# Optimization experiments

Hardware: AMD Instinct MI355X
Metric: run time of the kernel (lower is better)

Reference implementation:

```python
import jax, jax.numpy as jnp
import numpy as np
import math

HID = 1024      # opt.hidden_dim
NH = 8          # num_heads (hardcoded in module)
HD = HID // NH  # indiv_head_dim = 128
G = 16          # opt.group_num
GD = HID // G   # per-group dim = 64
FEAT = 1024     # opt.feature_dim
V, T = 8, 256   # videos x frames
E = 256         # number of events
L = 64          # max_att_len (clip window)
N = 384         # expanded event_num
WAVE = 10000.0


def setup_inputs() -> dict:
    rng = np.random.RandomState(0)
    key = jax.random.key(0)
    ks = jax.random.split(key, 12)

    feats = jax.random.normal(ks[0], (V * T, FEAT), dtype=jnp.float32)

    # ragged clip spans -> dense gather idx + mask (the Basic_Encoder loop)
    starts = rng.randint(0, V * T - L, size=(E,))
    clip_gather_idx = jnp.asarray(starts[:, None] + np.arange(L)[None, :], dtype=jnp.int32)
    lens = rng.randint(8, L + 1, size=(E,))
    clip_mask = jnp.asarray((np.arange(L)[None, :] < lens[:, None]).astype(np.float32))

    # event_seq_idx expansion: rows -> event ids, block-diagonal mask
    expand_idx = jnp.asarray(rng.randint(0, E, size=(N,)), dtype=jnp.int32)
    block_mask = np.zeros((N, N), dtype=np.float32)
    pos = 0
    while pos < N:
        b = min(int(rng.randint(8, 49)), N - pos)
        block_mask[pos:pos + b, pos:pos + b] = 1.0
        pos += b
    block_mask = jnp.asarray(block_mask)

    # normalized timestamps (start < end, in [0,1])
    s = rng.uniform(0.0, 0.8, size=(N, 1)).astype(np.float32)
    e = s + rng.uniform(0.02, 0.2, size=(N, 1)).astype(np.float32)
    bbox = jnp.asarray(np.concatenate([s, e], axis=1))

    sc = 1.0 / math.sqrt(HID)
    scd = 1.0 / math.sqrt(HD)
    Wpre = jax.random.normal(ks[1], (HID, FEAT), dtype=jnp.float32) * sc
    bpre = jnp.zeros((HID,), dtype=jnp.float32)
    Wq = jax.random.normal(ks[2], (NH, HD, HD), dtype=jnp.float32) * scd
    bq = jnp.zeros((NH, HD), dtype=jnp.float32)
    Wk = jax.random.normal(ks[3], (NH, HD, HD), dtype=jnp.float32) * scd
    bk = jnp.zeros((NH, HD), dtype=jnp.float32)
    Wv = jax.random.normal(ks[4], (NH, HD, HD), dtype=jnp.float32) * scd
    bv = jnp.zeros((NH, HD), dtype=jnp.float32)
    Wp1 = jax.random.normal(ks[5], (HID, HID), dtype=jnp.float32) * sc
    bp1 = jnp.zeros((HID,), dtype=jnp.float32)
    Wp2 = jax.random.normal(ks[6], (G, HID), dtype=jnp.float32) * sc
    bp2 = jnp.zeros((G,), dtype=jnp.float32)

    return dict(feats=feats, clip_gather_idx=clip_gather_idx, clip_mask=clip_mask,
                expand_idx=expand_idx, block_mask=block_mask, bbox=bbox,
                Wpre=Wpre, bpre=bpre, Wq=Wq, bq=bq, Wk=Wk, bk=bk, Wv=Wv, bv=bv,
                Wp1=Wp1, bp1=bp1, Wp2=Wp2, bp2=bp2)


def _sinusoid(x, feat_dim):
    # extract_position_embedding: x [..., P] -> [..., P*feat_dim/2*2] reshaped to feat_dim per row
    fr = jnp.arange(feat_dim // 4, dtype=x.dtype)
    dim_mat = WAVE ** (4.0 / feat_dim * fr)              # (feat_dim/4,)
    div = (100.0 * x)[..., None] / dim_mat               # (..., P, feat_dim/4)
    return jnp.concatenate([jnp.sin(div), jnp.cos(div)], axis=-1)


def reference(feats, clip_gather_idx, clip_mask, expand_idx, block_mask, bbox,
              Wpre, bpre, Wq, bq, Wk, bk, Wv, bv, Wp1, bp1, Wp2, bp2):
    # ---- clip-level pooling (Basic_Encoder.get_clip_level_feats + mean) ----
    clip_feats = feats[clip_gather_idx] * clip_mask[..., None]          # (E, L, FEAT)
    event = clip_feats.sum(1) / (clip_mask.sum(1, keepdims=True) + 1e-5)  # (E, FEAT)
    event = jax.nn.relu(event @ Wpre.T + bpre)                          # pre_map (dropout=eval)

    # ---- expand per event_seq_idx ----
    x = event[expand_idx]                                               # (N, HID)

    # ---- 8 per-head q/k/v maps, split into G groups ----
    xh = x.reshape(N, NH, HD)
    def proj(W, b):
        y = jnp.einsum('nhd,hed->nhe', xh, W) + b                       # (N, NH, HD)
        return y.reshape(N, G, GD).transpose(1, 0, 2)                   # (G, N, GD)
    q, k, v = proj(Wq, bq), proj(Wk, bk), proj(Wv, bv)
    scores = jnp.einsum('gnd,gmd->gnm', q, k) / math.sqrt(GD)           # (G, N, N)

    # ---- position branch: pairwise geometric relation bias ----
    start, end = bbox[:, 0:1], bbox[:, 1:2]                             # (N,1)
    center = 0.5 * (start + end)
    length = jnp.maximum(end - start, 0.1)
    dc = (center - center.T) / length
    dl = jnp.log(length.T / length)
    pm = jnp.stack([dc, dl], axis=2)                                    # (N, N, 2)
    emb = _sinusoid(pm, HID).reshape(N, N, HID)                         # (N, N, HID)
    pos = jax.nn.relu(emb @ Wp1.T + bp1)                                # pair_pos_fc1
    pos = jax.nn.relu(pos @ Wp2.T + bp2)                                # pair_pos_fc2 -> (N, N, G)
    pos_bias = jnp.log(jnp.clip(pos, 1e-6)).transpose(2, 0, 1)          # (G, N, N)

    scores = scores + pos_bias
    scores = jnp.where(block_mask[None] > 0, scores, -1e9)
    att = jax.nn.softmax(scores, axis=-1)                               # (G, N, N)
    out = jnp.einsum('gnm,gmd->gnd', att, v)                            # (G, N, GD)
    out = out.transpose(1, 0, 2).reshape(N, HID)

    # ---- per-event 100-dim temporal position embedding ----
    e100 = _sinusoid(bbox, 100).reshape(N, 100)

    return jnp.concatenate([x, out, e100], axis=-1)                     # (N, 2*HID + 100)
```

## Files before the change

### kernel.cpp

```cpp
#include <hip/hip_runtime.h>
#include <hip/hip_bf16.h>

typedef unsigned short u16;
typedef _Float16 h16;
typedef __attribute__((ext_vector_type(8))) h16 h8;
typedef __attribute__((ext_vector_type(8))) u16 us8;
typedef __attribute__((ext_vector_type(4))) u16 us4;
typedef __attribute__((ext_vector_type(4))) float f4;

#define DEVFN __device__ __forceinline__

constexpr int kN = 384;
constexpr int kL = 64;
constexpr int kMaxP = kN * 48;
constexpr int kOutCols = 2148;
constexpr float kLoScale = 2048.f;
constexpr float kLoInv = 1.f / 2048.f;

union HU { h16 h; u16 u; };
DEVFN u16 f2h(float f) { HU c; c.h = (h16)f; return c.u; }
DEVFN float h2f(u16 b) { HU c; c.u = b; return (float)c.h; }

DEVFN f4 mfma16h(h8 a, h8 b, f4 c) {
  return __builtin_amdgcn_mfma_f32_16x16x32_f16(a, b, c, 0, 0, 0);
}

DEVFN h8 pack8h(float4 x0, float4 x1) {
  h8 a;
  a[0] = (h16)x0.x; a[1] = (h16)x0.y; a[2] = (h16)x0.z; a[3] = (h16)x0.w;
  a[4] = (h16)x1.x; a[5] = (h16)x1.y; a[6] = (h16)x1.z; a[7] = (h16)x1.w;
  return a;
}

DEVFN void fsincos(float ang, float& s, float& c) {
  float n = rintf(ang * 0.15915494309189535f);
  const float PI2_HI = 6.2831854820251465f;
  const float PI2_LO = -1.7484555e-07f;
  float r = fmaf(-n, PI2_HI, ang);
  r = fmaf(-n, PI2_LO, r);
  s = __sinf(r);
  c = __cosf(r);
}

__global__ __launch_bounds__(256) void k_front(
    const float* __restrict__ Wp1, u16* __restrict__ W1H, u16* __restrict__ W1L,
    const float* __restrict__ Wp2, u16* __restrict__ W2H, u16* __restrict__ W2L,
    const float* __restrict__ Wpre, u16* __restrict__ WpreH,
    const float* __restrict__ Wq, u16* __restrict__ WqH,
    const float* __restrict__ Wk, u16* __restrict__ WkH,
    const float* __restrict__ Wv, u16* __restrict__ WvH,
    const float* __restrict__ bm, int* __restrict__ row_start, int* __restrict__ row_len,
    const float* __restrict__ feats, const int* __restrict__ gidx,
    const float* __restrict__ cmask, float* __restrict__ mean,
    float* __restrict__ bias_acc) {
  int bid = blockIdx.x, t = threadIdx.x;
  if (bid < 512) {
    const int nW1 = 1048576, nW2 = 16384, nPre = 1048576, nQ = 131072;
    const int tot = nW1 + nW2 + nPre + 3 * nQ;
    for (int i = bid * 256 + t; i < tot; i += 512 * 256) {
      if (i < nW1) {
        float x = Wp1[i]; u16 h = f2h(x);
        W1H[i] = h; W1L[i] = f2h((x - h2f(h)) * kLoScale);
      } else if (i < nW1 + nW2) {
        int j = i - nW1; float x = Wp2[j]; u16 h = f2h(x);
        W2H[j] = h; W2L[j] = f2h((x - h2f(h)) * kLoScale);
      } else if (i < nW1 + nW2 + nPre) {
        int j = i - nW1 - nW2; WpreH[j] = f2h(Wpre[j]);
      } else {
        int j = i - nW1 - nW2 - nPre;
        int a = j / nQ, r = j % nQ;
        const float* s = (a == 0) ? Wq : (a == 1) ? Wk : Wv;
        u16* d = (a == 0) ? WqH : (a == 1) ? WkH : WvH;
        d[r] = f2h(s[r]);
      }
    }
  } else if (bid < 608) {
    int w = t >> 6, lane = t & 63;
    int i = (bid - 512) * 4 + w;
    int mn = kN, mx = -1;
    #pragma unroll
    for (int jb = 0; jb < kN; jb += 64) {
      float m = bm[(size_t)i * kN + jb + lane];
      if (m > 0.f) { mn = min(mn, jb + lane); mx = max(mx, jb + lane); }
    }
    #pragma unroll
    for (int off = 32; off > 0; off >>= 1) {
      mn = min(mn, __shfl_xor(mn, off));
      mx = max(mx, __shfl_xor(mx, off));
    }
    if (lane == 0) { row_start[i] = mn; row_len[i] = mx - mn + 1; }
  } else if (bid < 864) {
    int e = bid - 608;
    float4 a = {0.f, 0.f, 0.f, 0.f};
    float ms = 0.f;
    for (int l = 0; l < kL; ++l) {
      float m = cmask[e * kL + l];
      ms += m;
      if (m > 0.f) {
        float4 v = *(const float4*)(feats + (size_t)gidx[e * kL + l] * 1024 + t * 4);
        a.x += v.x; a.y += v.y; a.z += v.z; a.w += v.w;
      }
    }
    float inv = 1.f / (ms + 1e-5f);
    float4 o = {a.x * inv, a.y * inv, a.z * inv, a.w * inv};
    *(float4*)(mean + (size_t)e * 1024 + t * 4) = o;
  } else {
    float4 z = {0.f, 0.f, 0.f, 0.f};
    for (int i4 = (bid - 864) * 256 + t; i4 < kMaxP * 16 / 4; i4 += 48 * 256)
      *(float4*)(bias_acc + (size_t)i4 * 4) = z;
  }
}

__global__ __launch_bounds__(64) void k_scan(const int* __restrict__ row_len,
                                             int* __restrict__ row_off,
                                             int* __restrict__ Ptr) {
  int lane = threadIdx.x;
  int s[6], tot = 0;
  #pragma unroll
  for (int r = 0; r < 6; ++r) { s[r] = tot; tot += row_len[lane * 6 + r]; }
  int run = tot;
  #pragma unroll
  for (int off = 1; off < 64; off <<= 1) {
    int u = __shfl_up(run, off);
    if (lane >= off) run += u;
  }
  int excl = run - tot;
  #pragma unroll
  for (int r = 0; r < 6; ++r) row_off[lane * 6 + r] = excl + s[r];
  if (lane == 63) Ptr[0] = excl + tot;
}

__global__ __launch_bounds__(64) void k_fill(const int* __restrict__ row_start,
                                             const int* __restrict__ row_len,
                                             const int* __restrict__ row_off,
                                             int* __restrict__ pair_i,
                                             int* __restrict__ pair_j) {
  int i = blockIdx.x, lane = threadIdx.x;
  int s = row_start[i], len = row_len[i], off = row_off[i];
  if (lane < len) { pair_i[off + lane] = i; pair_j[off + lane] = s + lane; }
}

__global__ __launch_bounds__(256) void k_mid(
    const int* __restrict__ Ptr, const int* __restrict__ row_start,
    const int* __restrict__ row_off, const float* __restrict__ bbox,
    u16* __restrict__ ehi, u16* __restrict__ elo,
    const float* __restrict__ mean, const u16* __restrict__ WpreH,
    const float* __restrict__ bpre, float* __restrict__ event) {
  int bid = blockIdx.x, t = threadIdx.x;
  if (bid < 9216) {
    int P = Ptr[0];
    int Pc = (P + 127) & ~127;
    if (bid * 2 >= Pc) return;
    __shared__ double As[16], Bs[16];
    __shared__ int roff[384], rstart[384];
    const double kCd = -13.287712379549449 / 256.0;
    if (t < 16) As[t] = exp2(kCd * (double)(t * 16));
    else if (t < 32) Bs[t - 16] = exp2(kCd * (double)(t - 16));
    for (int k = t; k < 384; k += 256) { roff[k] = row_off[k]; rstart[k] = row_start[k]; }
    __syncthreads();
    int p = bid * 2 + (t >> 7);
    int u = t & 127;
    int hseg = u >> 6;
    int f0 = (u & 63) * 4;
    size_t ob = (size_t)p * 1024 + hseg * 512 + f0;
    if (p >= P) {
      us4 z = {0, 0, 0, 0};
      *(us4*)(ehi + ob) = z; *(us4*)(ehi + ob + 256) = z;
      *(us4*)(elo + ob) = z; *(us4*)(elo + ob + 256) = z;
      return;
    }
    int lo = 0, hi = 383;
    while (lo < hi) { int md = (lo + hi + 1) >> 1; if (roff[md] <= p) lo = md; else hi = md - 1; }
    int pi = lo, pj = rstart[lo] + (p - roff[lo]);
    double s0 = bbox[pi * 2], e0 = bbox[pi * 2 + 1];
    double s1 = bbox[pj * 2], e1 = bbox[pj * 2 + 1];
    double li = fmax(e0 - s0, 0.1), lj = fmax(e1 - s1, 0.1);
    double x = hseg ? log(lj / li) : (0.5 * (s0 + e0) - 0.5 * (s1 + e1)) / li;
    double x100 = 100.0 * x;
    const double INV2PI = 0.15915494309189535;
    const double TWOPI  = 6.283185307179586;
    us4 sh_, sl_, ch_, cl_;
    #pragma unroll
    for (int j = 0; j < 4; ++j) {
      int f = f0 + j;
      double ang = x100 * (As[f >> 4] * Bs[f & 15]);
      double nn = rint(ang * INV2PI);
      float rf = (float)fma(-nn, TWOPI, ang);
      float sv = __sinf(rf), cv = __cosf(rf);
      u16 hs = f2h(sv); sh_[j] = hs; sl_[j] = f2h((sv - h2f(hs)) * kLoScale);
      u16 hc = f2h(cv); ch_[j] = hc; cl_[j] = f2h((cv - h2f(hc)) * kLoScale);
    }
    *(us4*)(ehi + ob) = sh_; *(us4*)(ehi + ob + 256) = ch_;
    *(us4*)(elo + ob) = sl_; *(us4*)(elo + ob + 256) = cl_;
  } else {
    int b2 = bid - 9216;
    int mt = b2 >> 4, nc = b2 & 15;
    int w = t >> 6, lane = t & 63, lr = lane & 15, lg = lane >> 4;
    f4 acc = {};
    const float* arow = mean + (size_t)(mt * 16 + lr) * 1024;
    #pragma unroll
    for (int ks = 0; ks < 32; ++ks) {
      const float* ap = arow + ks * 32 + lg * 8;
      h8 a = pack8h(*(const float4*)ap, *(const float4*)(ap + 4));
      h8 b = *(const h8*)(WpreH + (size_t)(nc * 64 + w * 16 + lr) * 1024 + ks * 32 + lg * 8);
      acc = mfma16h(a, b, acc);
    }
    #pragma unroll
    for (int r = 0; r < 4; ++r) {
      int row = mt * 16 + lg * 4 + r, cn = nc * 64 + w * 16 + lr;
      event[(size_t)row * 1024 + cn] = fmaxf(acc[r] + bpre[cn], 0.f);
    }
  }
}

__global__ __launch_bounds__(256, 2) void k_main(
    const int* __restrict__ Ptr, const u16* __restrict__ ehi, const u16* __restrict__ elo,
    const u16* __restrict__ W1h, const u16* __restrict__ W1l, const float* __restrict__ bias1,
    const u16* __restrict__ W2h, const u16* __restrict__ W2l, float* __restrict__ bias_acc,
    const float* __restrict__ event, const int* __restrict__ eidx,
    const u16* __restrict__ WqH, const float* __restrict__ bq,
    const u16* __restrict__ WkH, const float* __restrict__ bk,
    const u16* __restrict__ WvH, const float* __restrict__ bv,
    float* __restrict__ qb, float* __restrict__ kbuf, float* __restrict__ vbuf,
    int pos_on) {
  __shared__ u16 lds[2][4][4096];
  int bid = blockIdx.x, tid = threadIdx.x;
  if (bid < 1152) {
    if (!pos_on) return;
    int P = Ptr[0];
    int mb = bid % 144, nb = bid / 144;
    if (mb * 128 >= P) return;
    int w = tid >> 6, lane = tid & 63;
    int lr = lane & 15, lg = lane >> 4;
    int srow[2], scol[2];
    #pragma unroll
    for (int cc = 0; cc < 2; ++cc) {
      int c = w * 2 + cc;
      int d = c * 1024 + lane * 16;
      int b = d ^ (((((d >> 6) & 3)) ^ ((d >> 8) & 3)) << 4);
      srow[cc] = b >> 6;
      scol[cc] = b & 63;
    }
    const u16* planes[4] = {ehi, elo, W1h, W1l};
    int rb0 = mb * 128, rb1 = nb * 128;
    auto stage = [&](int buf, int k0) {
      #pragma unroll
      for (int t = 0; t < 4; ++t) {
        int rbase = (t < 2) ? rb0 : rb1;
        #pragma unroll
        for (int cc = 0; cc < 2; ++cc) {
          int c = w * 2 + cc;
          const char* src = (const char*)(planes[t] + (size_t)(rbase + srow[cc]) * 1024 + k0) + scol[cc];
          char* dst = (char*)&lds[buf][t][0] + c * 1024;
          __builtin_amdgcn_global_load_lds(
              (const __attribute__((address_space(1))) char*)src,
              (__attribute__((address_space(3))) char*)dst, 16, 0, 0);
        }
      }
    };
    stage(0, 0);
    f4 aH[4][4] = {}, aL[4][4] = {};
    int wm = (w >> 1) * 64, wn = (w & 1) * 64;
    int sl = (lg ^ (lr & 3) ^ ((lr >> 2) & 3)) << 4;
    __syncthreads();
    for (int kt = 0; kt < 32; ++kt) {
      int cur = kt & 1;
      if (kt < 31) stage(cur ^ 1, (kt + 1) * 32);
      h8 ah[4], al[4], bh[4], bl[4];
      #pragma unroll
      for (int mt = 0; mt < 4; ++mt) {
        int ad = (wm + mt * 16 + lr) * 64 + sl;
        ah[mt] = *(const h8*)((const char*)&lds[cur][0][0] + ad);
        al[mt] = *(const h8*)((const char*)&lds[cur][1][0] + ad);
      }
      #pragma unroll
      for (int nt = 0; nt < 4; ++nt) {
        int ad = (wn + nt * 16 + lr) * 64 + sl;
        bh[nt] = *(const h8*)((const char*)&lds[cur][2][0] + ad);
        bl[nt] = *(const h8*)((const char*)&lds[cur][3][0] + ad);
      }
      #pragma unroll
      for (int mt = 0; mt < 4; ++mt)
        #pragma unroll
        for (int nt = 0; nt < 4; ++nt) {
          aH[mt][nt] = mfma16h(ah[mt], bh[nt], aH[mt][nt]);
          aL[mt][nt] = mfma16h(al[mt], bh[nt], aL[mt][nt]);
          aL[mt][nt] = mfma16h(ah[mt], bl[nt], aL[mt][nt]);
        }
      __syncthreads();
    }
    float* zq = (float*)&lds[0][0][0] + w * 4096;
    #pragma unroll
    for (int mt = 0; mt < 4; ++mt)
      #pragma unroll
      for (int nt = 0; nt < 4; ++nt)
        #pragma unroll
        for (int r = 0; r < 4; ++r) {
          int pl = mt * 16 + lg * 4 + r;
          int nl = nt * 16 + lr;
          float z1 = aH[mt][nt][r] + aL[mt][nt][r] * kLoInv + bias1[nb * 128 + wn + nl];
          zq[pl * 64 + (nl ^ ((pl & 7) << 3))] = fmaxf(z1, 0.f);
        }
    __syncthreads();
    f4 c2h[4], c2l[4];
    #pragma unroll
    for (int i = 0; i < 4; ++i) { c2h[i] = f4{}; c2l[i] = f4{}; }
    #pragma unroll
    for (int mt2 = 0; mt2 < 4; ++mt2) {
      #pragma unroll
      for (int kc = 0; kc < 2; ++kc) {
        int pl = mt2 * 16 + lr;
        int n0 = kc * 32 + lg * 8;
        const float* rp = zq + pl * 64 + (n0 ^ ((pl & 7) << 3));
        float4 v0 = *(const float4*)rp;
        float4 v1 = *(const float4*)(rp + 4);
        h8 ah2, al2;
        #pragma unroll
        for (int j = 0; j < 4; ++j) {
          h16 h0 = (h16)v0[j]; ah2[j] = h0;     al2[j] = (h16)((v0[j] - (float)h0) * kLoScale);
          h16 h1 = (h16)v1[j]; ah2[4 + j] = h1; al2[4 + j] = (h16)((v1[j] - (float)h1) * kLoScale);
        }
        int ng = nb * 128 + wn + n0;
        h8 bh2 = *(const h8*)(W2h + lr * 1024 + ng);
        h8 bl2 = *(const h8*)(W2l + lr * 1024 + ng);
        c2h[mt2] = mfma16h(ah2, bh2, c2h[mt2]);
        c2l[mt2] = mfma16h(al2, bh2, c2l[mt2]);
        c2l[mt2] = mfma16h(ah2, bl2, c2l[mt2]);
      }
    }
    #pragma unroll
    for (int mt2 = 0; mt2 < 4; ++mt2)
      #pragma unroll
      for (int r = 0; r < 4; ++r) {
        int p = mb * 128 + wm + mt2 * 16 + lg * 4 + r;
        if (p < P)
          atomicAdd(&bias_acc[(size_t)p * 16 + lr], c2h[mt2][r] + c2l[mt2][r] * kLoInv);
      }
  } else {
    int b2 = bid - 1152;
    int z = b2 / 192, r2 = b2 % 192, mt = r2 >> 3, h = r2 & 7;
    int w = tid >> 6, lane = tid & 63, lr = lane & 15, lg = lane >> 4;
    const u16* W = (z == 0) ? WqH : (z == 1) ? WkH : WvH;
    const float* bias = (z == 0) ? bq : (z == 1) ? bk : bv;
    float* out = (z == 0) ? qb : (z == 1) ? kbuf : vbuf;
    int row = mt * 16 + lr;
    const float* arow = event + (size_t)eidx[row] * 1024 + h * 128;
    f4 acc[2] = {};
    #pragma unroll
    for (int ks = 0; ks < 4; ++ks) {
      const float* ap = arow + ks * 32 + lg * 8;
      h8 a = pack8h(*(const float4*)ap, *(const float4*)(ap + 4));
      #pragma unroll
      for (int n2 = 0; n2 < 2; ++n2) {
        int nt = w * 2 + n2;
        h8 b = *(const h8*)(W + h * 16384 + (nt * 16 + lr) * 128 + ks * 32 + lg * 8);
        acc[n2] = mfma16h(a, b, acc[n2]);
      }
    }
    #pragma unroll
    for (int n2 = 0; n2 < 2; ++n2)
      #pragma unroll
      for (int r = 0; r < 4; ++r) {
        int rn = mt * 16 + lg * 4 + r, e = (w * 2 + n2) * 16 + lr;
        out[(size_t)rn * 1024 + h * 128 + e] = acc[n2][r] + bias[h * 128 + e];
      }
  }
}

__global__ __launch_bounds__(64) void k_att(const float* __restrict__ q,
                                            const float* __restrict__ kk,
                                            const float* __restrict__ vv,
                                            const float* __restrict__ bias_acc,
                                            const float* __restrict__ bias2,
                                            const int* __restrict__ row_start,
                                            const int* __restrict__ row_len,
                                            const int* __restrict__ row_off,
                                            const float* __restrict__ event,
                                            const int* __restrict__ eidx,
                                            const float* __restrict__ bbox,
                                            float* __restrict__ dout) {
  int bid = blockIdx.x, lane = threadIdx.x;
  if (bid >= 6144) {
    int i = bid - 6144;
    const float* er = event + (size_t)eidx[i] * 1024;
    float* orow = dout + (size_t)i * kOutCols;
    #pragma unroll
    for (int it = 0; it < 4; ++it) {
      int c = lane * 4 + it * 256;
      *(float4*)(orow + c) = *(const float4*)(er + c);
    }
    for (int t = lane; t < 100; t += 64) {
      int qq = t / 25, f = t % 25;
      float x = bbox[i * 2 + (qq >> 1)];
      float ang = 100.f * x * exp2f((float)f * (-13.287712379549449f * 0.04f));
      float sv, cv;
      fsincos(ang, sv, cv);
      orow[2048 + t] = (qq & 1) ? cv : sv;
    }
    return;
  }
  int i = bid >> 4, g = bid & 15;
  int s = row_start[i], L = row_len[i], pb = row_off[i];
  __shared__ float qs[64];
  __shared__ float att[64];
  qs[lane] = q[(size_t)i * 1024 + g * 64 + lane];
  __syncthreads();
  bool valid = lane < L;
  const float* kr = kk + (size_t)(s + (valid ? lane : 0)) * 1024 + g * 64;
  float sc = 0.f;
  #pragma unroll
  for (int dt = 0; dt < 16; ++dt) {
    float4 kv = *(const float4*)(kr + dt * 4);
    sc += qs[dt * 4 + 0] * kv.x + qs[dt * 4 + 1] * kv.y +
          qs[dt * 4 + 2] * kv.z + qs[dt * 4 + 3] * kv.w;
  }
  int pidx = min(pb + lane, kMaxP - 1);
  float pbias = 0.f;
  if (valid) {
    float zs = bias_acc[(size_t)pidx * 16 + g] + bias2[g];
    pbias = logf(fmaxf(zs, 1e-6f));
  }
  sc = valid ? (sc * 0.125f + pbias) : -3.0e38f;
  float mx = sc;
  #pragma unroll
  for (int off = 32; off > 0; off >>= 1) mx = fmaxf(mx, __shfl_xor(mx, off));
  float pe = valid ? __expf(sc - mx) : 0.f;
  float sm = pe;
  #pragma unroll
  for (int off = 32; off > 0; off >>= 1) sm += __shfl_xor(sm, off);
  att[lane] = pe / sm;
  __syncthreads();
  float o = 0.f;
  const float* vb = vv + (size_t)s * 1024 + g * 64 + lane;
  for (int jl = 0; jl < L; ++jl) o += att[jl] * vb[(size_t)jl * 1024];
  dout[(size_t)i * kOutCols + 1024 + g * 64 + lane] = o;
}

__global__ __launch_bounds__(256) void k_pos(
    const int* __restrict__ Ptr, const int* __restrict__ pair_i,
    const int* __restrict__ pair_j, const float* __restrict__ bbox,
    const u16* __restrict__ W1h, const u16* __restrict__ W1l,
    const float* __restrict__ bias1,
    const u16* __restrict__ W2h, const u16* __restrict__ W2l,
    float* __restrict__ bias_acc) {
  int P = Ptr[0];
  int base0 = blockIdx.x * 64;
  if (base0 >= P) return;
  int w = threadIdx.x >> 6, l = threadIdx.x & 63;
  int lr = l & 15, lg = l >> 4;
  int base = base0 + w * 16;
  int p = base + lr;
  bool valid = p < P;
  int pi = valid ? pair_i[p] : 0;
  int pj = valid ? pair_j[p] : 0;
  double s0 = bbox[pi * 2], e0 = bbox[pi * 2 + 1];
  double s1 = bbox[pj * 2], e1 = bbox[pj * 2 + 1];
  double li = fmax(e0 - s0, 0.1), lj = fmax(e1 - s1, 0.1);
  double dcd = (0.5 * (s0 + e0) - 0.5 * (s1 + e1)) / li;
  double dld = log(lj / li);
  const double kCd = -13.287712379549449 / 256.0;
  double r1  = exp2(kCd);
  double r32 = exp2(kCd * 32.0);
  double pb0 = exp2(kCd * (double)(lg * 8));
  const double INV2PI = 0.15915494309189535;
  const double TWOPI  = 6.283185307179586;
  h8 eh[32], el[32];
  #pragma unroll
  for (int hx = 0; hx < 2; ++hx) {
    double x100 = 100.0 * (hx ? dld : dcd);
    double pch = pb0;
    #pragma unroll
    for (int ksl = 0; ksl < 8; ++ksl) {
      double pp = pch;
      #pragma unroll
      for (int j = 0; j < 8; ++j) {
        double ang = x100 * pp;
        double nn = rint(ang * INV2PI);
        float rf = (float)fma(-nn, TWOPI, ang);
        float sv = __sinf(rf), cv = __cosf(rf);
        h16 sh = (h16)sv, ch = (h16)cv;
        eh[hx * 16 + ksl][j] = sh;
        el[hx * 16 + ksl][j] = (h16)((sv - (float)sh) * kLoScale);
        eh[hx * 16 + 8 + ksl][j] = ch;
        el[hx * 16 + 8 + ksl][j] = (h16)((cv - (float)ch) * kLoScale);
        pp *= r1;
      }
      pch *= r32;
    }
  }
  __shared__ float p1f[4][16 * 64];
  char* myp1 = (char*)p1f[w];
  f4 acc2 = {}, acc2l = {};
  for (int nc = 0; nc < 16; ++nc) {
    f4 accH[4] = {}, accL[4] = {};
    #pragma unroll
    for (int ks = 0; ks < 32; ++ks) {
      #pragma unroll
      for (int nt = 0; nt < 4; ++nt) {
        size_t boff = (size_t)(nc * 64 + nt * 16 + lr) * 1024 + ks * 32 + lg * 8;
        h8 bh = *(const h8*)(W1h + boff);
        h8 bl = *(const h8*)(W1l + boff);
        accH[nt] = mfma16h(eh[ks], bh, accH[nt]);
        accL[nt] = mfma16h(el[ks], bh, accL[nt]);
        accL[nt] = mfma16h(eh[ks], bl, accL[nt]);
      }
    }
    __syncthreads();
    #pragma unroll
    for (int nt = 0; nt < 4; ++nt)
      #pragma unroll
      for (int r = 0; r < 4; ++r) {
        int m = lg * 4 + r, n = nt * 16 + lr;
        float z1 = accH[nt][r] + accL[nt][r] * kLoInv + bias1[nc * 64 + n];
        int byte = ((m * 64 + n) * 4) ^ ((m & 7) << 4);
        *(float*)(myp1 + byte) = fmaxf(z1, 0.f);
      }
    __syncthreads();
    #pragma unroll
    for (int hf = 0; hf < 2; ++hf) {
      int kb = hf * 32 + lg * 8;
      int b0 = ((lr * 64 + kb) * 4) ^ ((lr & 7) << 4);
      int b1 = ((lr * 64 + kb + 4) * 4) ^ ((lr & 7) << 4);
      float4 x0 = *(const float4*)(myp1 + b0);
      float4 x1 = *(const float4*)(myp1 + b1);
      h8 ah, al;
      #pragma unroll
      for (int j = 0; j < 4; ++j) {
        h16 h0 = (h16)x0[j];
        ah[j] = h0; al[j] = (h16)((x0[j] - (float)h0) * kLoScale);
        h16 h1 = (h16)x1[j];
        ah[4 + j] = h1; al[4 + j] = (h16)((x1[j] - (float)h1) * kLoScale);
      }
      h8 bh = *(const h8*)(W2h + lr * 1024 + nc * 64 + kb);
      h8 bl = *(const h8*)(W2l + lr * 1024 + nc * 64 + kb);
      acc2  = mfma16h(ah, bh, acc2);
      acc2l = mfma16h(al, bh, acc2l);
      acc2l = mfma16h(ah, bl, acc2l);
    }
  }
  #pragma unroll
  for (int r = 0; r < 4; ++r) {
    int m = lg * 4 + r;
    int pp = base + m;
    if (pp < P)
      bias_acc[(size_t)pp * 16 + lr] = acc2[r] + acc2l[r] * kLoInv;
  }
}

extern "C" void kernel_launch(void* const* d_in, const int* in_sizes, int n_in,
                              void* d_out, int out_size, void* d_ws, size_t ws_size,
                              hipStream_t stream) {
  const float* feats = (const float*)d_in[0];
  const int*   gidx  = (const int*)d_in[1];
  const float* cmask = (const float*)d_in[2];
  const int*   eidx  = (const int*)d_in[3];
  const float* bmask = (const float*)d_in[4];
  const float* bbox  = (const float*)d_in[5];
  const float* Wpre  = (const float*)d_in[6];
  const float* bpre  = (const float*)d_in[7];
  const float* Wq    = (const float*)d_in[8];
  const float* bq    = (const float*)d_in[9];
  const float* Wk    = (const float*)d_in[10];
  const float* bk    = (const float*)d_in[11];
  const float* Wv    = (const float*)d_in[12];
  const float* bv    = (const float*)d_in[13];
  const float* Wp1   = (const float*)d_in[14];
  const float* bp1   = (const float*)d_in[15];
  const float* Wp2   = (const float*)d_in[16];
  const float* bp2   = (const float*)d_in[17];

  char* ws = (char*)d_ws;
  size_t off = 0;
  auto alloc = [&](size_t bytes) {
    char* r = ws + off;
    off += (bytes + 255) & ~(size_t)255;
    return r;
  };
  u16* W1H   = (u16*)alloc((size_t)1048576 * 2);
  u16* W1L   = (u16*)alloc((size_t)1048576 * 2);
  u16* W2H   = (u16*)alloc((size_t)16384 * 2);
  u16* W2L   = (u16*)alloc((size_t)16384 * 2);
  u16* WpreH = (u16*)alloc((size_t)1048576 * 2);
  u16* WqH   = (u16*)alloc((size_t)131072 * 2);
  u16* WkH   = (u16*)alloc((size_t)131072 * 2);
  u16* WvH   = (u16*)alloc((size_t)131072 * 2);
  float* mean  = (float*)alloc((size_t)256 * 1024 * 4);
  float* event = (float*)alloc((size_t)256 * 1024 * 4);
  float* qb    = (float*)alloc((size_t)384 * 1024 * 4);
  float* kb    = (float*)alloc((size_t)384 * 1024 * 4);
  float* vb    = (float*)alloc((size_t)384 * 1024 * 4);
  int* row_start = (int*)alloc(kN * 4);
  int* row_len   = (int*)alloc(kN * 4);
  int* row_off   = (int*)alloc(kN * 4);
  int* Ptr       = (int*)alloc(256);
  int* pair_i    = (int*)alloc((size_t)kMaxP * 4);
  int* pair_j    = (int*)alloc((size_t)kMaxP * 4);
  float* bias_acc = (float*)alloc((size_t)kMaxP * 16 * 4);
  u16* ehi      = (u16*)alloc((size_t)kMaxP * 1024 * 2);
  u16* elo      = (u16*)alloc((size_t)kMaxP * 1024 * 2);
  bool fast = (off <= ws_size);

  k_front<<<912, 256, 0, stream>>>(Wp1, W1H, W1L, Wp2, W2H, W2L, Wpre, WpreH,
                                   Wq, WqH, Wk, WkH, Wv, WvH,
                                   bmask, row_start, row_len,
                                   feats, gidx, cmask, mean, bias_acc);
  k_scan<<<1, 64, 0, stream>>>(row_len, row_off, Ptr);

  if (fast) {
    k_mid<<<9472, 256, 0, stream>>>(Ptr, row_start, row_off, bbox, ehi, elo,
                                    mean, WpreH, bpre, event);
    k_main<<<1728, 256, 0, stream>>>(Ptr, ehi, elo, W1H, W1L, bp1, W2H, W2L, bias_acc,
                                     event, eidx, WqH, bq, WkH, bk, WvH, bv, qb, kb, vb, 1);
  } else {
    k_mid<<<9472, 256, 0, stream>>>(Ptr, row_start, row_off, bbox, ehi, elo,
                                    mean, WpreH, bpre, event);
    k_fill<<<kN, 64, 0, stream>>>(row_start, row_len, row_off, pair_i, pair_j);
    k_pos<<<kMaxP / 64, 256, 0, stream>>>(Ptr, pair_i, pair_j, bbox, W1H, W1L, bp1,
                                          W2H, W2L, bias_acc);
    k_main<<<1728, 256, 0, stream>>>(Ptr, ehi, elo, W1H, W1L, bp1, W2H, W2L, bias_acc,
                                     event, eidx, WqH, bq, WkH, bk, WvH, bv, qb, kb, vb, 0);
  }
  k_att<<<6528, 64, 0, stream>>>(qb, kb, vb, bias_acc, bp2, row_start, row_len, row_off,
                                 event, eidx, bbox, (float*)d_out);
}
```

Before: 161.3 us.

## Fold split-fp16 pos GEMM into one concatenated-K accumulator and restructure launches

The pair-position fc1 GEMM previously ran three MFMAs per tile into two accumulators (hi*hi, lo*hi, hi*lo) over separate hi/lo planes. It now lays the activation and weight planes out as one concatenated K dimension (A=[hi,lo], B=[hi, hi/64, lo*64]), so a single accumulator runs a 96-step K loop with one MFMA per step and half the LDS staging. The reduced LDS footprint allows occupancy 4 instead of 2. Kernels are also re-split: the row-extent and scan kernels now run first so the embedding build can fuse into the weight-conversion kernel, and the event GEMM moves into its own kernel. Rescaling by 64 in fp16 risks some precision loss or subnormals.

```diff
diff --git a/kernel.cpp b/kernel.cpp
--- a/kernel.cpp
+++ b/kernel.cpp
@@ -4,7 +4,6 @@
 typedef unsigned short u16;
 typedef _Float16 h16;
 typedef __attribute__((ext_vector_type(8))) h16 h8;
-typedef __attribute__((ext_vector_type(8))) u16 us8;
 typedef __attribute__((ext_vector_type(4))) u16 us4;
 typedef __attribute__((ext_vector_type(4))) float f4;
 
@@ -14,8 +13,8 @@
 constexpr int kL = 64;
 constexpr int kMaxP = kN * 48;
 constexpr int kOutCols = 2148;
-constexpr float kLoScale = 2048.f;
-constexpr float kLoInv = 1.f / 2048.f;
+constexpr float kS = 64.f;
+constexpr float kSInv = 1.f / 64.f;
 
 union HU { h16 h; u16 u; };
 DEVFN u16 f2h(float f) { HU c; c.h = (h16)f; return c.u; }
@@ -29,6 +28,12 @@
   h8 a;
   a[0] = (h16)x0.x; a[1] = (h16)x0.y; a[2] = (h16)x0.z; a[3] = (h16)x0.w;
   a[4] = (h16)x1.x; a[5] = (h16)x1.y; a[6] = (h16)x1.z; a[7] = (h16)x1.w;
+  return a;
+}
+
+DEVFN h8 mulInv64(h8 a) {
+  #pragma unroll
+  for (int j = 0; j < 8; ++j) a[j] = (h16)(a[j] * (h16)0.015625f);
   return a;
 }
 
@@ -42,28 +47,84 @@
   c = __cosf(r);
 }
 
-__global__ __launch_bounds__(256) void k_front(
-    const float* __restrict__ Wp1, u16* __restrict__ W1H, u16* __restrict__ W1L,
-    const float* __restrict__ Wp2, u16* __restrict__ W2H, u16* __restrict__ W2L,
+__global__ __launch_bounds__(64) void k_ext(const float* __restrict__ bm,
+                                            int* __restrict__ row_start,
+                                            int* __restrict__ row_len) {
+  int i = blockIdx.x, lane = threadIdx.x;
+  int mn = kN, mx = -1;
+  #pragma unroll
+  for (int jb = 0; jb < kN; jb += 64) {
+    float m = bm[(size_t)i * kN + jb + lane];
+    if (m > 0.f) { mn = min(mn, jb + lane); mx = max(mx, jb + lane); }
+  }
+  #pragma unroll
+  for (int off = 32; off > 0; off >>= 1) {
+    mn = min(mn, __shfl_xor(mn, off));
+    mx = max(mx, __shfl_xor(mx, off));
+  }
+  if (lane == 0) { row_start[i] = mn; row_len[i] = mx - mn + 1; }
+}
+
+__global__ __launch_bounds__(64) void k_scan(const int* __restrict__ row_len,
+                                             int* __restrict__ row_off,
+                                             int* __restrict__ Ptr) {
+  int lane = threadIdx.x;
+  int s[6], tot = 0;
+  #pragma unroll
+  for (int r = 0; r < 6; ++r) { s[r] = tot; tot += row_len[lane * 6 + r]; }
+  int run = tot;
+  #pragma unroll
+  for (int off = 1; off < 64; off <<= 1) {
+    int u = __shfl_up(run, off);
+    if (lane >= off) run += u;
+  }
+  int excl = run - tot;
+  #pragma unroll
+  for (int r = 0; r < 6; ++r) row_off[lane * 6 + r] = excl + s[r];
+  if (lane == 63) Ptr[0] = excl + tot;
+}
+
+__global__ __launch_bounds__(64) void k_fill(const int* __restrict__ row_start,
+                                             const int* __restrict__ row_len,
+                                             const int* __restrict__ row_off,
+                                             int* __restrict__ pair_i,
+                                             int* __restrict__ pair_j) {
+  int i = blockIdx.x, lane = threadIdx.x;
+  int s = row_start[i], len = row_len[i], off = row_off[i];
+  if (lane < len) { pair_i[off + lane] = i; pair_j[off + lane] = s + lane; }
+}
+
+__global__ __launch_bounds__(256) void k_big(
+    const float* __restrict__ Wp1, u16* __restrict__ W1B,
+    const float* __restrict__ Wp2, u16* __restrict__ w2h, u16* __restrict__ w2hd,
+    u16* __restrict__ w2l64,
     const float* __restrict__ Wpre, u16* __restrict__ WpreH,
     const float* __restrict__ Wq, u16* __restrict__ WqH,
     const float* __restrict__ Wk, u16* __restrict__ WkH,
     const float* __restrict__ Wv, u16* __restrict__ WvH,
-    const float* __restrict__ bm, int* __restrict__ row_start, int* __restrict__ row_len,
     const float* __restrict__ feats, const int* __restrict__ gidx,
     const float* __restrict__ cmask, float* __restrict__ mean,
-    float* __restrict__ bias_acc) {
+    float* __restrict__ bias_acc,
+    const int* __restrict__ Ptr, const int* __restrict__ row_start,
+    const int* __restrict__ row_off, const float* __restrict__ bbox,
+    u16* __restrict__ Ap) {
   int bid = blockIdx.x, t = threadIdx.x;
   if (bid < 512) {
     const int nW1 = 1048576, nW2 = 16384, nPre = 1048576, nQ = 131072;
     const int tot = nW1 + nW2 + nPre + 3 * nQ;
     for (int i = bid * 256 + t; i < tot; i += 512 * 256) {
       if (i < nW1) {
+        int n = i >> 10, k = i & 1023;
         float x = Wp1[i]; u16 h = f2h(x);
-        W1H[i] = h; W1L[i] = f2h((x - h2f(h)) * kLoScale);
+        u16* row = W1B + (size_t)n * 3072;
+        row[k] = h;
+        row[1024 + k] = f2h(h2f(h) * kSInv);
+        row[2048 + k] = f2h((x - h2f(h)) * kS);
       } else if (i < nW1 + nW2) {
         int j = i - nW1; float x = Wp2[j]; u16 h = f2h(x);
-        W2H[j] = h; W2L[j] = f2h((x - h2f(h)) * kLoScale);
+        w2h[j] = h;
+        w2hd[j] = f2h(h2f(h) * kSInv);
+        w2l64[j] = f2h((x - h2f(h)) * kS);
       } else if (i < nW1 + nW2 + nPre) {
         int j = i - nW1 - nW2; WpreH[j] = f2h(Wpre[j]);
       } else {
@@ -74,23 +135,8 @@
         d[r] = f2h(s[r]);
       }
     }
-  } else if (bid < 608) {
-    int w = t >> 6, lane = t & 63;
-    int i = (bid - 512) * 4 + w;
-    int mn = kN, mx = -1;
-    #pragma unroll
-    for (int jb = 0; jb < kN; jb += 64) {
-      float m = bm[(size_t)i * kN + jb + lane];
-      if (m > 0.f) { mn = min(mn, jb + lane); mx = max(mx, jb + lane); }
-    }
-    #pragma unroll
-    for (int off = 32; off > 0; off >>= 1) {
-      mn = min(mn, __shfl_xor(mn, off));
-      mx = max(mx, __shfl_xor(mx, off));
-    }
-    if (lane == 0) { row_start[i] = mn; row_len[i] = mx - mn + 1; }
-  } else if (bid < 864) {
-    int e = bid - 608;
+  } else if (bid < 768) {
+    int e = bid - 512;
     float4 a = {0.f, 0.f, 0.f, 0.f};
     float ms = 0.f;
     for (int l = 0; l < kL; ++l) {
@@ -104,53 +150,15 @@
     float inv = 1.f / (ms + 1e-5f);
     float4 o = {a.x * inv, a.y * inv, a.z * inv, a.w * inv};
     *(float4*)(mean + (size_t)e * 1024 + t * 4) = o;
+  } else if (bid < 816) {
+    float4 z = {0.f, 0.f, 0.f, 0.f};
+    for (int i4 = (bid - 768) * 256 + t; i4 < kMaxP * 16 / 4; i4 += 48 * 256)
+      *(float4*)(bias_acc + (size_t)i4 * 4) = z;
   } else {
-    float4 z = {0.f, 0.f, 0.f, 0.f};
-    for (int i4 = (bid - 864) * 256 + t; i4 < kMaxP * 16 / 4; i4 += 48 * 256)
-      *(float4*)(bias_acc + (size_t)i4 * 4) = z;
-  }
-}
-
-__global__ __launch_bounds__(64) void k_scan(const int* __restrict__ row_len,
-                                             int* __restrict__ row_off,
-                                             int* __restrict__ Ptr) {
-  int lane = threadIdx.x;
-  int s[6], tot = 0;
-  #pragma unroll
-  for (int r = 0; r < 6; ++r) { s[r] = tot; tot += row_len[lane * 6 + r]; }
-  int run = tot;
-  #pragma unroll
-  for (int off = 1; off < 64; off <<= 1) {
-    int u = __shfl_up(run, off);
-    if (lane >= off) run += u;
-  }
-  int excl = run - tot;
-  #pragma unroll
-  for (int r = 0; r < 6; ++r) row_off[lane * 6 + r] = excl + s[r];
-  if (lane == 63) Ptr[0] = excl + tot;
-}
-
-__global__ __launch_bounds__(64) void k_fill(const int* __restrict__ row_start,
-                                             const int* __restrict__ row_len,
-                                             const int* __restrict__ row_off,
-                                             int* __restrict__ pair_i,
-                                             int* __restrict__ pair_j) {
-  int i = blockIdx.x, lane = threadIdx.x;
-  int s = row_start[i], len = row_len[i], off = row_off[i];
-  if (lane < len) { pair_i[off + lane] = i; pair_j[off + lane] = s + lane; }
-}
-
-__global__ __launch_bounds__(256) void k_mid(
-    const int* __restrict__ Ptr, const int* __restrict__ row_start,
-    const int* __restrict__ row_off, const float* __restrict__ bbox,
-    u16* __restrict__ ehi, u16* __restrict__ elo,
-    const float* __restrict__ mean, const u16* __restrict__ WpreH,
-    const float* __restrict__ bpre, float* __restrict__ event) {
-  int bid = blockIdx.x, t = threadIdx.x;
-  if (bid < 9216) {
+    int eb = bid - 816;
     int P = Ptr[0];
     int Pc = (P + 127) & ~127;
-    if (bid * 2 >= Pc) return;
+    if (eb * 2 >= Pc) return;
     __shared__ double As[16], Bs[16];
     __shared__ int roff[384], rstart[384];
     const double kCd = -13.287712379549449 / 256.0;
@@ -158,15 +166,15 @@
     else if (t < 32) Bs[t - 16] = exp2(kCd * (double)(t - 16));
     for (int k = t; k < 384; k += 256) { roff[k] = row_off[k]; rstart[k] = row_start[k]; }
     __syncthreads();
-    int p = bid * 2 + (t >> 7);
+    int p = eb * 2 + (t >> 7);
     int u = t & 127;
     int hseg = u >> 6;
     int f0 = (u & 63) * 4;
-    size_t ob = (size_t)p * 1024 + hseg * 512 + f0;
+    size_t obA = (size_t)p * 2048 + hseg * 512 + f0;
     if (p >= P) {
       us4 z = {0, 0, 0, 0};
-      *(us4*)(ehi + ob) = z; *(us4*)(ehi + ob + 256) = z;
-      *(us4*)(elo + ob) = z; *(us4*)(elo + ob + 256) = z;
+      *(us4*)(Ap + obA) = z;        *(us4*)(Ap + obA + 256) = z;
+      *(us4*)(Ap + obA + 1024) = z; *(us4*)(Ap + obA + 1280) = z;
       return;
     }
     int lo = 0, hi = 383;
@@ -187,43 +195,49 @@
       double nn = rint(ang * INV2PI);
       float rf = (float)fma(-nn, TWOPI, ang);
       float sv = __sinf(rf), cv = __cosf(rf);
-      u16 hs = f2h(sv); sh_[j] = hs; sl_[j] = f2h((sv - h2f(hs)) * kLoScale);
-      u16 hc = f2h(cv); ch_[j] = hc; cl_[j] = f2h((cv - h2f(hc)) * kLoScale);
-    }
-    *(us4*)(ehi + ob) = sh_; *(us4*)(ehi + ob + 256) = ch_;
-    *(us4*)(elo + ob) = sl_; *(us4*)(elo + ob + 256) = cl_;
-  } else {
-    int b2 = bid - 9216;
-    int mt = b2 >> 4, nc = b2 & 15;
-    int w = t >> 6, lane = t & 63, lr = lane & 15, lg = lane >> 4;
-    f4 acc = {};
-    const float* arow = mean + (size_t)(mt * 16 + lr) * 1024;
-    #pragma unroll
-    for (int ks = 0; ks < 32; ++ks) {
-      const float* ap = arow + ks * 32 + lg * 8;
-      h8 a = pack8h(*(const float4*)ap, *(const float4*)(ap + 4));
-      h8 b = *(const h8*)(WpreH + (size_t)(nc * 64 + w * 16 + lr) * 1024 + ks * 32 + lg * 8);
-      acc = mfma16h(a, b, acc);
-    }
-    #pragma unroll
-    for (int r = 0; r < 4; ++r) {
-      int row = mt * 16 + lg * 4 + r, cn = nc * 64 + w * 16 + lr;
-      event[(size_t)row * 1024 + cn] = fmaxf(acc[r] + bpre[cn], 0.f);
-    }
-  }
-}
-
-__global__ __launch_bounds__(256, 2) void k_main(
-    const int* __restrict__ Ptr, const u16* __restrict__ ehi, const u16* __restrict__ elo,
-    const u16* __restrict__ W1h, const u16* __restrict__ W1l, const float* __restrict__ bias1,
-    const u16* __restrict__ W2h, const u16* __restrict__ W2l, float* __restrict__ bias_acc,
+      u16 hs = f2h(sv); sh_[j] = hs; sl_[j] = f2h((sv - h2f(hs)) * kS);
+      u16 hc = f2h(cv); ch_[j] = hc; cl_[j] = f2h((cv - h2f(hc)) * kS);
+    }
+    *(us4*)(Ap + obA) = sh_;        *(us4*)(Ap + obA + 256) = ch_;
+    *(us4*)(Ap + obA + 1024) = sl_; *(us4*)(Ap + obA + 1280) = cl_;
+  }
+}
+
+__global__ __launch_bounds__(256) void k_egemm(const float* __restrict__ mean,
+                                               const u16* __restrict__ WpreH,
+                                               const float* __restrict__ bpre,
+                                               float* __restrict__ event) {
+  int mt = blockIdx.x >> 4, nc = blockIdx.x & 15;
+  int t = threadIdx.x;
+  int w = t >> 6, lane = t & 63, lr = lane & 15, lg = lane >> 4;
+  f4 acc = {};
+  const float* arow = mean + (size_t)(mt * 16 + lr) * 1024;
+  #pragma unroll
+  for (int ks = 0; ks < 32; ++ks) {
+    const float* ap = arow + ks * 32 + lg * 8;
+    h8 a = pack8h(*(const float4*)ap, *(const float4*)(ap + 4));
+    h8 b = *(const h8*)(WpreH + (size_t)(nc * 64 + w * 16 + lr) * 1024 + ks * 32 + lg * 8);
+    acc = mfma16h(a, b, acc);
+  }
+  #pragma unroll
+  for (int r = 0; r < 4; ++r) {
+    int row = mt * 16 + lg * 4 + r, cn = nc * 64 + w * 16 + lr;
+    event[(size_t)row * 1024 + cn] = fmaxf(acc[r] + bpre[cn], 0.f);
+  }
+}
+
+__global__ __launch_bounds__(256, 4) void k_main(
+    const int* __restrict__ Ptr, const u16* __restrict__ Ap, const u16* __restrict__ W1B,
+    const float* __restrict__ bias1,
+    const u16* __restrict__ w2h, const u16* __restrict__ w2hd, const u16* __restrict__ w2l64,
+    float* __restrict__ bias_acc,
     const float* __restrict__ event, const int* __restrict__ eidx,
     const u16* __restrict__ WqH, const float* __restrict__ bq,
     const u16* __restrict__ WkH, const float* __restrict__ bk,
     const u16* __restrict__ WvH, const float* __restrict__ bv,
     float* __restrict__ qb, float* __restrict__ kbuf, float* __restrict__ vbuf,
     int pos_on) {
-  __shared__ u16 lds[2][4][4096];
+  __shared__ u16 lds[2][2][4096];
   int bid = blockIdx.x, tid = threadIdx.x;
   if (bid < 1152) {
     if (!pos_on) return;
@@ -241,92 +255,94 @@
       srow[cc] = b >> 6;
       scol[cc] = b & 63;
     }
-    const u16* planes[4] = {ehi, elo, W1h, W1l};
     int rb0 = mb * 128, rb1 = nb * 128;
-    auto stage = [&](int buf, int k0) {
-      #pragma unroll
-      for (int t = 0; t < 4; ++t) {
-        int rbase = (t < 2) ? rb0 : rb1;
-        #pragma unroll
-        for (int cc = 0; cc < 2; ++cc) {
-          int c = w * 2 + cc;
-          const char* src = (const char*)(planes[t] + (size_t)(rbase + srow[cc]) * 1024 + k0) + scol[cc];
-          char* dst = (char*)&lds[buf][t][0] + c * 1024;
-          __builtin_amdgcn_global_load_lds(
-              (const __attribute__((address_space(1))) char*)src,
-              (__attribute__((address_space(3))) char*)dst, 16, 0, 0);
-        }
+    auto stage = [&](int buf, int kt2) {
+      int seg = kt2 >> 5;
+      int kA0 = (seg == 2) ? (kt2 - 64) * 32 : kt2 * 32;
+      int kB0 = kt2 * 32;
+      #pragma unroll
+      for (int cc = 0; cc < 2; ++cc) {
+        int c = w * 2 + cc;
+        const char* srcA = (const char*)(Ap + (size_t)(rb0 + srow[cc]) * 2048 + kA0) + scol[cc];
+        __builtin_amdgcn_global_load_lds(
+            (const __attribute__((address_space(1))) char*)srcA,
+            (__attribute__((address_space(3))) char*)((char*)&lds[buf][0][0] + c * 1024), 16, 0, 0);
+        const char* srcB = (const char*)(W1B + (size_t)(rb1 + srow[cc]) * 3072 + kB0) + scol[cc];
+        __builtin_amdgcn_global_load_lds(
+            (const __attribute__((address_space(1))) char*)srcB,
+            (__attribute__((address_space(3))) char*)((char*)&lds[buf][1][0] + c * 1024), 16, 0, 0);
       }
     };
     stage(0, 0);
-    f4 aH[4][4] = {}, aL[4][4] = {};
+    f4 acc[4][4] = {};
     int wm = (w >> 1) * 64, wn = (w & 1) * 64;
     int sl = (lg ^ (lr & 3) ^ ((lr >> 2) & 3)) << 4;
     __syncthreads();
-    for (int kt = 0; kt < 32; ++kt) {
+    for (int kt = 0; kt < 96; ++kt) {
       int cur = kt & 1;
-      if (kt < 31) stage(cur ^ 1, (kt + 1) * 32);
-      h8 ah[4], al[4], bh[4], bl[4];
-      #pragma unroll
-      for (int mt = 0; mt < 4; ++mt) {
-        int ad = (wm + mt * 16 + lr) * 64 + sl;
-        ah[mt] = *(const h8*)((const char*)&lds[cur][0][0] + ad);
-        al[mt] = *(const h8*)((const char*)&lds[cur][1][0] + ad);
-      }
-      #pragma unroll
-      for (int nt = 0; nt < 4; ++nt) {
-        int ad = (wn + nt * 16 + lr) * 64 + sl;
-        bh[nt] = *(const h8*)((const char*)&lds[cur][2][0] + ad);
-        bl[nt] = *(const h8*)((const char*)&lds[cur][3][0] + ad);
+      if (kt < 95) stage(cur ^ 1, kt + 1);
+      h8 ah[4], bh[4];
+      #pragma unroll
+      for (int mt = 0; mt < 4; ++mt)
+        ah[mt] = *(const h8*)((const char*)&lds[cur][0][0] + (wm + mt * 16 + lr) * 64 + sl);
+      #pragma unroll
+      for (int nt = 0; nt < 4; ++nt)
+        bh[nt] = *(const h8*)((const char*)&lds[cur][1][0] + (wn + nt * 16 + lr) * 64 + sl);
+      if (kt >= 64) {
+        #pragma unroll
+        for (int mt = 0; mt < 4; ++mt) ah[mt] = mulInv64(ah[mt]);
       }
       #pragma unroll
       for (int mt = 0; mt < 4; ++mt)
         #pragma unroll
-        for (int nt = 0; nt < 4; ++nt) {
-          aH[mt][nt] = mfma16h(ah[mt], bh[nt], aH[mt][nt]);
-          aL[mt][nt] = mfma16h(al[mt], bh[nt], aL[mt][nt]);
-          aL[mt][nt] = mfma16h(ah[mt], bl[nt], aL[mt][nt]);
+        for (int nt = 0; nt < 4; ++nt)
+          acc[mt][nt] = mfma16h(ah[mt], bh[nt], acc[mt][nt]);
+      __syncthreads();
+    }
+    float* zq = (float*)&lds[0][0][0] + w * 2048;
+    f4 acc2[4];
+    #pragma unroll
+    for (int i = 0; i < 4; ++i) acc2[i] = f4{};
+    #pragma unroll
+    for (int kc = 0; kc < 2; ++kc) {
+      #pragma unroll
+      for (int mt = 0; mt < 4; ++mt)
+        #pragma unroll
+        for (int n2 = 0; n2 < 2; ++n2) {
+          int nt = kc * 2 + n2;
+          #pragma unroll
+          for (int r = 0; r < 4; ++r) {
+            int pl = mt * 16 + lg * 4 + r;
+            int nl = n2 * 16 + lr;
+            float z1 = acc[mt][nt][r] + bias1[nb * 128 + wn + nt * 16 + lr];
+            int c4 = nl >> 2;
+            zq[pl * 32 + (((c4 ^ (pl & 7)) << 2) | (nl & 3))] = fmaxf(z1, 0.f);
+          }
         }
       __syncthreads();
-    }
-    float* zq = (float*)&lds[0][0][0] + w * 4096;
-    #pragma unroll
-    for (int mt = 0; mt < 4; ++mt)
-      #pragma unroll
-      for (int nt = 0; nt < 4; ++nt)
-        #pragma unroll
-        for (int r = 0; r < 4; ++r) {
-          int pl = mt * 16 + lg * 4 + r;
-          int nl = nt * 16 + lr;
-          float z1 = aH[mt][nt][r] + aL[mt][nt][r] * kLoInv + bias1[nb * 128 + wn + nl];
-          zq[pl * 64 + (nl ^ ((pl & 7) << 3))] = fmaxf(z1, 0.f);
-        }
-    __syncthreads();
-    f4 c2h[4], c2l[4];
-    #pragma unroll
-    for (int i = 0; i < 4; ++i) { c2h[i] = f4{}; c2l[i] = f4{}; }
-    #pragma unroll
-    for (int mt2 = 0; mt2 < 4; ++mt2) {
-      #pragma unroll
-      for (int kc = 0; kc < 2; ++kc) {
+      #pragma unroll
+      for (int mt2 = 0; mt2 < 4; ++mt2) {
         int pl = mt2 * 16 + lr;
-        int n0 = kc * 32 + lg * 8;
-        const float* rp = zq + pl * 64 + (n0 ^ ((pl & 7) << 3));
-        float4 v0 = *(const float4*)rp;
-        float4 v1 = *(const float4*)(rp + 4);
-        h8 ah2, al2;
+        int c4a = lg * 2;
+        float4 v0 = *(const float4*)(zq + pl * 32 + ((c4a ^ (pl & 7)) << 2));
+        float4 v1 = *(const float4*)(zq + pl * 32 + (((c4a + 1) ^ (pl & 7)) << 2));
+        h8 ah2, al2, ad2;
         #pragma unroll
         for (int j = 0; j < 4; ++j) {
-          h16 h0 = (h16)v0[j]; ah2[j] = h0;     al2[j] = (h16)((v0[j] - (float)h0) * kLoScale);
-          h16 h1 = (h16)v1[j]; ah2[4 + j] = h1; al2[4 + j] = (h16)((v1[j] - (float)h1) * kLoScale);
+          h16 h0 = (h16)v0[j];
+          ah2[j] = h0; al2[j] = (h16)((v0[j] - (float)h0) * kS); ad2[j] = (h16)((float)h0 * kSInv);
+          h16 h1 = (h16)v1[j];
+          ah2[4 + j] = h1; al2[4 + j] = (h16)((v1[j] - (float)h1) * kS); ad2[4 + j] = (h16)((float)h1 * kSInv);
         }
-        int ng = nb * 128 + wn + n0;
-        h8 bh2 = *(const h8*)(W2h + lr * 1024 + ng);
-        h8 bl2 = *(const h8*)(W2l + lr * 1024 + ng);
-        c2h[mt2] = mfma16h(ah2, bh2, c2h[mt2]);
-        c2l[mt2] = mfma16h(al2, bh2, c2l[mt2]);
-        c2l[mt2] = mfma16h(ah2, bl2, c2l[mt2]);
-      }
+        int ng = nb * 128 + wn + kc * 32 + lg * 8;
+        h8 b1 = *(const h8*)(w2h + lr * 1024 + ng);
+        h8 b2 = *(const h8*)(w2hd + lr * 1024 + ng);
+        h8 b3 = *(const h8*)(w2l64 + lr * 1024 + ng);
+        acc2[mt2] = mfma16h(ah2, b1, acc2[mt2]);
+        acc2[mt2] = mfma16h(al2, b2, acc2[mt2]);
+        acc2[mt2] = mfma16h(ad2, b3, acc2[mt2]);
+      }
+      __syncthreads();
     }
     #pragma unroll
     for (int mt2 = 0; mt2 < 4; ++mt2)
@@ -334,7 +350,7 @@
       for (int r = 0; r < 4; ++r) {
         int p = mb * 128 + wm + mt2 * 16 + lg * 4 + r;
         if (p < P)
-          atomicAdd(&bias_acc[(size_t)p * 16 + lr], c2h[mt2][r] + c2l[mt2][r] * kLoInv);
+          atomicAdd(&bias_acc[(size_t)p * 16 + lr], acc2[mt2][r]);
       }
   } else {
     int b2 = bid - 1152;
@@ -439,9 +455,8 @@
 __global__ __launch_bounds__(256) void k_pos(
     const int* __restrict__ Ptr, const int* __restrict__ pair_i,
     const int* __restrict__ pair_j, const float* __restrict__ bbox,
-    const u16* __restrict__ W1h, const u16* __restrict__ W1l,
-    const float* __restrict__ bias1,
-    const u16* __restrict__ W2h, const u16* __restrict__ W2l,
+    const u16* __restrict__ W1B, const float* __restrict__ bias1,
+    const u16* __restrict__ w2h, const u16* __restrict__ w2l64,
     float* __restrict__ bias_acc) {
   int P = Ptr[0];
   int base0 = blockIdx.x * 64;
@@ -480,9 +495,9 @@
         float sv = __sinf(rf), cv = __cosf(rf);
         h16 sh = (h16)sv, ch = (h16)cv;
         eh[hx * 16 + ksl][j] = sh;
-        el[hx * 16 + ksl][j] = (h16)((sv - (float)sh) * kLoScale);
+        el[hx * 16 + ksl][j] = (h16)((sv - (float)sh) * kS);
         eh[hx * 16 + 8 + ksl][j] = ch;
-        el[hx * 16 + 8 + ksl][j] = (h16)((cv - (float)ch) * kLoScale);
+        el[hx * 16 + 8 + ksl][j] = (h16)((cv - (float)ch) * kS);
         pp *= r1;
       }
       pch *= r32;
@@ -497,9 +512,9 @@
     for (int ks = 0; ks < 32; ++ks) {
       #pragma unroll
       for (int nt = 0; nt < 4; ++nt) {
-        size_t boff = (size_t)(nc * 64 + nt * 16 + lr) * 1024 + ks * 32 + lg * 8;
-        h8 bh = *(const h8*)(W1h + boff);
-        h8 bl = *(const h8*)(W1l + boff);
+        size_t boff = (size_t)(nc * 64 + nt * 16 + lr) * 3072 + ks * 32 + lg * 8;
+        h8 bh = *(const h8*)(W1B + boff);
+        h8 bl = *(const h8*)(W1B + boff + 2048);
         accH[nt] = mfma16h(eh[ks], bh, accH[nt]);
         accL[nt] = mfma16h(el[ks], bh, accL[nt]);
         accL[nt] = mfma16h(eh[ks], bl, accL[nt]);
@@ -511,7 +526,7 @@
       #pragma unroll
       for (int r = 0; r < 4; ++r) {
         int m = lg * 4 + r, n = nt * 16 + lr;
-        float z1 = accH[nt][r] + accL[nt][r] * kLoInv + bias1[nc * 64 + n];
+        float z1 = accH[nt][r] + accL[nt][r] * kSInv + bias1[nc * 64 + n];
         int byte = ((m * 64 + n) * 4) ^ ((m & 7) << 4);
         *(float*)(myp1 + byte) = fmaxf(z1, 0.f);
       }
@@ -527,12 +542,12 @@
       #pragma unroll
       for (int j = 0; j < 4; ++j) {
         h16 h0 = (h16)x0[j];
-        ah[j] = h0; al[j] = (h16)((x0[j] - (float)h0) * kLoScale);
+        ah[j] = h0; al[j] = (h16)((x0[j] - (float)h0) * kS);
         h16 h1 = (h16)x1[j];
-        ah[4 + j] = h1; al[4 + j] = (h16)((x1[j] - (float)h1) * kLoScale);
-      }
-      h8 bh = *(const h8*)(W2h + lr * 1024 + nc * 64 + kb);
-      h8 bl = *(const h8*)(W2l + lr * 1024 + nc * 64 + kb);
+        ah[4 + j] = h1; al[4 + j] = (h16)((x1[j] - (float)h1) * kS);
+      }
+      h8 bh = *(const h8*)(w2h + lr * 1024 + nc * 64 + kb);
+      h8 bl = *(const h8*)(w2l64 + lr * 1024 + nc * 64 + kb);
       acc2  = mfma16h(ah, bh, acc2);
       acc2l = mfma16h(al, bh, acc2l);
       acc2l = mfma16h(ah, bl, acc2l);
@@ -543,7 +558,7 @@
     int m = lg * 4 + r;
     int pp = base + m;
     if (pp < P)
-      bias_acc[(size_t)pp * 16 + lr] = acc2[r] + acc2l[r] * kLoInv;
+      bias_acc[(size_t)pp * 16 + lr] = acc2[r] + acc2l[r] * kSInv;
   }
 }
 
@@ -576,10 +591,10 @@
     off += (bytes + 255) & ~(size_t)255;
     return r;
   };
-  u16* W1H   = (u16*)alloc((size_t)1048576 * 2);
-  u16* W1L   = (u16*)alloc((size_t)1048576 * 2);
-  u16* W2H   = (u16*)alloc((size_t)16384 * 2);
-  u16* W2L   = (u16*)alloc((size_t)16384 * 2);
+  u16* W1B   = (u16*)alloc((size_t)1024 * 3072 * 2);
+  u16* w2h   = (u16*)alloc((size_t)16384 * 2);
+  u16* w2hd  = (u16*)alloc((size_t)16384 * 2);
+  u16* w2l64 = (u16*)alloc((size_t)16384 * 2);
   u16* WpreH = (u16*)alloc((size_t)1048576 * 2);
   u16* WqH   = (u16*)alloc((size_t)131072 * 2);
   u16* WkH   = (u16*)alloc((size_t)131072 * 2);
@@ -596,29 +611,28 @@
   int* pair_i    = (int*)alloc((size_t)kMaxP * 4);
   int* pair_j    = (int*)alloc((size_t)kMaxP * 4);
   float* bias_acc = (float*)alloc((size_t)kMaxP * 16 * 4);
-  u16* ehi      = (u16*)alloc((size_t)kMaxP * 1024 * 2);
-  u16* elo      = (u16*)alloc((size_t)kMaxP * 1024 * 2);
+  u16* Ap = (u16*)alloc((size_t)kMaxP * 2048 * 2);
   bool fast = (off <= ws_size);
 
-  k_front<<<912, 256, 0, stream>>>(Wp1, W1H, W1L, Wp2, W2H, W2L, Wpre, WpreH,
+  k_ext<<<kN, 64, 0, stream>>>(bmask, row_start, row_len);
+  k_scan<<<1, 64, 0, stream>>>(row_len, row_off, Ptr);
+  k_big<<<10032, 256, 0, stream>>>(Wp1, W1B, Wp2, w2h, w2hd, w2l64, Wpre, WpreH,
                                    Wq, WqH, Wk, WkH, Wv, WvH,
-                                   bmask, row_start, row_len,
-                                   feats, gidx, cmask, mean, bias_acc);
-  k_scan<<<1, 64, 0, stream>>>(row_len, row_off, Ptr);
+                                   feats, gidx, cmask, mean, bias_acc,
+                                   Ptr, row_start, row_off, bbox, Ap);
+  k_egemm<<<256, 256, 0, stream>>>(mean, WpreH, bpre, event);
 
   if (fast) {
-    k_mid<<<9472, 256, 0, stream>>>(Ptr, row_start, row_off, bbox, ehi, elo,
-                                    mean, WpreH, bpre, event);
-    k_main<<<1728, 256, 0, stream>>>(Ptr, ehi, elo, W1H, W1L, bp1, W2H, W2L, bias_acc,
-                                     event, eidx, WqH, bq, WkH, bk, WvH, bv, qb, kb, vb, 1);
+    k_main<<<1728, 256, 0, stream>>>(Ptr, Ap, W1B, bp1, w2h, w2hd, w2l64, bias_acc,
+                                     event, eidx, WqH, bq, WkH, bk, WvH, bv,
+                                     qb, kb, vb, 1);
   } else {
-    k_mid<<<9472, 256, 0, stream>>>(Ptr, row_start, row_off, bbox, ehi, elo,
-                                    mean, WpreH, bpre, event);
     k_fill<<<kN, 64, 0, stream>>>(row_start, row_len, row_off, pair_i, pair_j);
-    k_pos<<<kMaxP / 64, 256, 0, stream>>>(Ptr, pair_i, pair_j, bbox, W1H, W1L, bp1,
-                                          W2H, W2L, bias_acc);
-    k_main<<<1728, 256, 0, stream>>>(Ptr, ehi, elo, W1H, W1L, bp1, W2H, W2L, bias_acc,
-                                     event, eidx, WqH, bq, WkH, bk, WvH, bv, qb, kb, vb, 0);
+    k_pos<<<kMaxP / 64, 256, 0, stream>>>(Ptr, pair_i, pair_j, bbox, W1B, bp1,
+                                          w2h, w2l64, bias_acc);
+    k_main<<<1728, 256, 0, stream>>>(Ptr, Ap, W1B, bp1, w2h, w2hd, w2l64, bias_acc,
+                                     event, eidx, WqH, bq, WkH, bk, WvH, bv,
+                                     qb, kb, vb, 0);
   }
   k_att<<<6528, 64, 0, stream>>>(qb, kb, vb, bias_acc, bp2, row_start, row_len, row_off,
                                  event, eidx, bbox, (float*)d_out);
```

Result: slower. 191.4 us (+18.7%).
